# Kernel optimization log

Hardware: AMD Instinct MI355X
Metric: run time of the kernel (lower is better)

## Reference

```python
import jax, jax.numpy as jnp
import numpy as np

N_ENT = 200000   # entity/relation vocab (shared, as code indexes both tables with same ids)
D = 256          # emb_dim
NB = 64          # max neighbors per entity
K = 21           # kernel_num
PROJ = 200       # project_num (hard-coded in module)
S = 5            # few-shot support size
Q = 1024         # query batch
PAD = N_ENT - 1  # padding_idx = len(rel_emb) - 1


def _kernel_mus(k):
    l = [1.0]
    b = 1.0 / (k - 1)
    l.append(1.0 - b / 2.0)
    for i in range(1, k - 1):
        l.append(l[i] - b)
    return np.asarray(l, np.float32)


def _kernel_sigmas(k):
    return np.asarray([0.001] + [0.1] * (k - 1), np.float32)


MU = jnp.asarray(_kernel_mus(K))        # [K]
SIGMA = jnp.asarray(_kernel_sigmas(K))  # [K]


def setup_inputs() -> dict:
    key = jax.random.key(0)
    ks = jax.random.split(key, 12)
    support_heads = jax.random.randint(ks[0], (S,), 0, N_ENT - 1)
    support_tails = jax.random.randint(ks[1], (S,), 0, N_ENT - 1)
    query_heads = jax.random.randint(ks[2], (Q,), 0, N_ENT - 1)
    query_tails = jax.random.randint(ks[3], (Q,), 0, N_ENT - 1)
    raw = jax.random.randint(ks[4], (N_ENT, NB, 2), 0, N_ENT - 1)
    pad_mask = jax.random.uniform(ks[5], (N_ENT, NB, 1)) < 0.2
    edge_data = jnp.where(pad_mask, PAD, raw).astype(jnp.int32)
    edge_nums = jnp.sum(edge_data[..., 1] != PAD, axis=1).astype(jnp.int32)
    rel_emb = jax.random.normal(ks[6], (N_ENT, D), jnp.float32) * 0.02
    ent_emb = jax.random.normal(ks[7], (N_ENT, D), jnp.float32) * 0.02
    sc = 1.0 / np.sqrt(D)
    attn_w = jax.random.normal(ks[8], (D, D), jnp.float32) * sc
    attn_b = jnp.zeros((D,), jnp.float32)
    d1_w = jax.random.normal(ks[9], (PROJ, K), jnp.float32) * (1.0 / np.sqrt(K))
    d1_b = jnp.zeros((PROJ,), jnp.float32)
    d2_w = jax.random.normal(ks[10], (1, PROJ), jnp.float32) * (1.0 / np.sqrt(PROJ))
    d2_b = jnp.zeros((1,), jnp.float32)
    return {
        'support_heads': support_heads, 'query_heads': query_heads,
        'support_tails': support_tails, 'query_tails': query_tails,
        'edge_data': edge_data, 'edge_nums': edge_nums,
        'rel_emb': rel_emb, 'ent_emb': ent_emb,
        'attn_w': attn_w, 'attn_b': attn_b,
        'd1_w': d1_w, 'd1_b': d1_b, 'd2_w': d2_w, 'd2_b': d2_b,
    }


def _l2norm(x):
    # F.normalize(x, 2, dim=-1): x / max(||x||, 1e-12)
    n = jnp.linalg.norm(x, axis=-1, keepdims=True)
    return x / jnp.maximum(n, 1e-12)


def reference(support_heads, query_heads, support_tails, query_tails,
              edge_data, edge_nums, rel_emb, ent_emb,
              attn_w, attn_b, d1_w, d1_b, d2_w, d2_b):
    # neighbor ids (column 1) and padding masks
    s_nb = edge_data[support_tails, :, 1]  # [S, NB]
    q_nb = edge_data[query_tails, :, 1]    # [Q, NB]
    mask_q = (q_nb != PAD).astype(jnp.float32)  # [Q, NB] (mask_s is unused in original)

    def attention(heads, tails, nb):
        t = ent_emb[tails] - ent_emb[heads]          # [B, D] relation-type embed
        t = t @ attn_w.T + attn_b                    # Linear(D, D)
        return jnp.einsum('bd,bnd->bn', t, ent_emb[nb])  # bmm similarity [B, NB]

    s_att = attention(support_heads, support_tails, s_nb)  # [S, NB]
    q_att = attention(query_heads, query_tails, q_nb)      # [Q, NB]

    s_e = _l2norm(rel_emb[s_nb])  # [S, NB, D]
    q_e = _l2norm(rel_emb[q_nb])  # [Q, NB, D]

    # vectorized over the original Python loop on support examples:
    sim = jnp.einsum('qnd,smd->sqnm', q_e, s_e)              # [S, Q, NBq, NBs]
    sim = sim * q_att[None, :, :, None] * s_att[:, None, None, :]
    pool = jnp.max(sim, axis=3)                               # topk(k=1, dim=2) -> [S, Q, NBq]
    pv = jnp.exp(-((pool[..., None] - MU) ** 2) / (SIGMA ** 2) / 2.0)  # [S, Q, NBq, K]
    logpv = jnp.log(jnp.clip(pv, 1e-30, None)) * mask_q[None, :, :, None] * 0.01
    tail_enc = jnp.sum(logpv, axis=2)                         # [S, Q, K]

    h = tail_enc @ d1_w.T + d1_b                              # [S, Q, PROJ]
    score = jax.nn.sigmoid(h @ d2_w.T + d2_b)[..., 0]         # [S, Q]
    return jnp.max(score, axis=0)                             # [Q]
```

## Files before the change

### kernel.cpp

```cpp
#include <hip/hip_runtime.h>
#include <hip/hip_bf16.h>
#include <math.h>

#define N_ENT 200000
#define DD 256
#define NB 64
#define NK 21
#define PROJ 200
#define NS 5
#define NQ 1024
#define PADID (N_ENT - 1)
#define LOGMIN -69.07755279f

typedef short s16x8 __attribute__((ext_vector_type(8)));
typedef float f32x4 __attribute__((ext_vector_type(4)));

__device__ inline unsigned short f2bf(float x) {
  __hip_bfloat16 h = __float2bfloat16(x);
  return __builtin_bit_cast(unsigned short, h);
}

__global__ __launch_bounds__(256) void k_transpose(const float* __restrict__ w,
                                                   float* __restrict__ wT) {
  int j = blockIdx.x, d = threadIdx.x;
  wT[j * DD + d] = w[d * DD + j];
}

__global__ __launch_bounds__(256) void k_t2(const int* __restrict__ qh, const int* __restrict__ qt,
                                            const int* __restrict__ sh, const int* __restrict__ st,
                                            const float* __restrict__ ent, const float* __restrict__ wT,
                                            const float* __restrict__ ab, float* __restrict__ t2) {
  int r = blockIdx.x, d = threadIdx.x;
  int head, tail;
  if (r < NQ) { head = qh[r]; tail = qt[r]; }
  else        { head = sh[r - NQ]; tail = st[r - NQ]; }
  __shared__ float tv[DD];
  tv[d] = ent[(size_t)tail * DD + d] - ent[(size_t)head * DD + d];
  __syncthreads();
  float acc = ab[d];
  #pragma unroll 8
  for (int j = 0; j < DD; ++j) acc += tv[j] * wT[j * DD + d];
  t2[r * DD + d] = acc;
}

__global__ __launch_bounds__(256) void k_qatt(const int* __restrict__ qt, const int* __restrict__ ed,
                                              const float* __restrict__ ent, const float* __restrict__ t2,
                                              float* __restrict__ qatt) {
  int q = blockIdx.x, tid = threadIdx.x;
  __shared__ float t2s[DD];
  __shared__ int nbs[NB];
  t2s[tid] = t2[q * DD + tid];
  if (tid < NB) nbs[tid] = ed[((size_t)qt[q] * NB + tid) * 2 + 1];
  __syncthreads();
  int n = tid >> 2, seg = tid & 3;
  const float4* er = (const float4*)(ent + (size_t)nbs[n] * DD + seg * 64);
  const float4* ts = (const float4*)(t2s + seg * 64);
  float s = 0.f;
  #pragma unroll
  for (int j = 0; j < 16; ++j) {
    float4 v = er[j], t = ts[j];
    s += v.x * t.x + v.y * t.y + v.z * t.z + v.w * t.w;
  }
  s += __shfl_xor(s, 1);
  s += __shfl_xor(s, 2);
  if (seg == 0) qatt[q * NB + n] = s;
}

__global__ __launch_bounds__(256) void k_support(const int* __restrict__ st, const int* __restrict__ ed,
                                                 const float* __restrict__ ent, const float* __restrict__ rel,
                                                 const float* __restrict__ t2,
                                                 unsigned short* __restrict__ Bb) {
  int s = blockIdx.x, tid = threadIdx.x;
  __shared__ float t2s[DD];
  __shared__ int nbs[NB];
  __shared__ float att[NB];
  t2s[tid] = t2[(NQ + s) * DD + tid];
  if (tid < NB) nbs[tid] = ed[((size_t)st[s] * NB + tid) * 2 + 1];
  __syncthreads();
  int n = tid >> 2, seg = tid & 3;
  const float4* er = (const float4*)(ent + (size_t)nbs[n] * DD + seg * 64);
  const float4* ts = (const float4*)(t2s + seg * 64);
  float a = 0.f;
  #pragma unroll
  for (int j = 0; j < 16; ++j) {
    float4 v = er[j], t = ts[j];
    a += v.x * t.x + v.y * t.y + v.z * t.z + v.w * t.w;
  }
  a += __shfl_xor(a, 1);
  a += __shfl_xor(a, 2);
  if (seg == 0) att[n] = a;
  const float4* rr = (const float4*)(rel + (size_t)nbs[n] * DD + seg * 64);
  float4 buf[16];
  float ss = 0.f;
  #pragma unroll
  for (int j = 0; j < 16; ++j) {
    float4 v = rr[j]; buf[j] = v;
    ss += v.x * v.x + v.y * v.y + v.z * v.z + v.w * v.w;
  }
  ss += __shfl_xor(ss, 1);
  ss += __shfl_xor(ss, 2);
  __syncthreads();
  float scale = att[n] / fmaxf(sqrtf(ss), 1e-12f);
  unsigned short* ob = Bb + ((size_t)s * NB + n) * DD + seg * 64;
  #pragma unroll
  for (int j = 0; j < 16; ++j) {
    float4 v = buf[j];
    ob[j * 4 + 0] = f2bf(v.x * scale);
    ob[j * 4 + 1] = f2bf(v.y * scale);
    ob[j * 4 + 2] = f2bf(v.z * scale);
    ob[j * 4 + 3] = f2bf(v.w * scale);
  }
}

#define AP 264
__global__ __launch_bounds__(256) void k_main(
    const int* __restrict__ qt, const int* __restrict__ ed,
    const float* __restrict__ rel, const unsigned short* __restrict__ Bg,
    const float* __restrict__ qatt,
    const float* __restrict__ d1w, const float* __restrict__ d1b,
    const float* __restrict__ d2w, const float* __restrict__ d2b,
    float* __restrict__ out) {
  int q = blockIdx.x, tid = threadIdx.x;
  int wv = tid >> 6, ln = tid & 63;
  int fr = ln & 15, kb = ln >> 4;

  __shared__ __align__(16) unsigned short As[NB * AP];
  __shared__ float pmax[NS][4][NB], pmin[NS][4][NB];
  __shared__ float att[NB], msk[NB], pol[NB], te[NK + 3], wred[4];
  __shared__ int nbs[NB];

  if (tid < NB) {
    int nb = ed[((size_t)qt[q] * NB + tid) * 2 + 1];
    nbs[tid] = nb;
    att[tid] = qatt[q * NB + tid];
    msk[tid] = (nb != PADID) ? 0.01f : 0.0f;
  }
  __syncthreads();
  {
    int n = tid >> 2, seg = tid & 3;
    const float4* rr = (const float4*)(rel + (size_t)nbs[n] * DD + seg * 64);
    float4 buf[16];
    float ss = 0.f;
    #pragma unroll
    for (int j = 0; j < 16; ++j) {
      float4 v = rr[j]; buf[j] = v;
      ss += v.x * v.x + v.y * v.y + v.z * v.z + v.w * v.w;
    }
    ss += __shfl_xor(ss, 1);
    ss += __shfl_xor(ss, 2);
    float inv = 1.0f / fmaxf(sqrtf(ss), 1e-12f);
    unsigned short* ap = As + n * AP + seg * 64;
    #pragma unroll
    for (int j = 0; j < 16; ++j) {
      float4 v = buf[j];
      unsigned int lo = (unsigned int)f2bf(v.x * inv) | ((unsigned int)f2bf(v.y * inv) << 16);
      unsigned int hi = (unsigned int)f2bf(v.z * inv) | ((unsigned int)f2bf(v.w * inv) << 16);
      *(unsigned int*)(ap + j * 4)     = lo;
      *(unsigned int*)(ap + j * 4 + 2) = hi;
    }
  }
  __syncthreads();

  f32x4 acc[4][5];
  #pragma unroll
  for (int i = 0; i < 4; ++i)
    #pragma unroll
    for (int j = 0; j < 5; ++j) acc[i][j] = (f32x4){0.f, 0.f, 0.f, 0.f};

  const unsigned short* abase = As + fr * AP + kb * 8;
  const unsigned short* bbase = Bg + ((size_t)(wv * 16 + fr)) * DD + kb * 8;

  s16x8 bcur[5], bnxt[5], afr[4];
  #pragma unroll
  for (int j = 0; j < 5; ++j) bcur[j] = *(const s16x8*)(bbase + (size_t)j * 64 * DD);
  #pragma unroll
  for (int k = 0; k < 8; ++k) {
    #pragma unroll
    for (int i = 0; i < 4; ++i) afr[i] = *(const s16x8*)(abase + i * 16 * AP + k * 32);
    if (k < 7) {
      #pragma unroll
      for (int j = 0; j < 5; ++j)
        bnxt[j] = *(const s16x8*)(bbase + (size_t)j * 64 * DD + (k + 1) * 32);
    }
    #pragma unroll
    for (int i = 0; i < 4; ++i)
      #pragma unroll
      for (int j = 0; j < 5; ++j)
        acc[i][j] = __builtin_amdgcn_mfma_f32_16x16x32_bf16(afr[i], bcur[j], acc[i][j], 0, 0, 0);
    #pragma unroll
    for (int j = 0; j < 5; ++j) bcur[j] = bnxt[j];
  }

  #pragma unroll
  for (int j = 0; j < 5; ++j) {
    #pragma unroll
    for (int i = 0; i < 4; ++i) {
      f32x4 mx = acc[i][j], mn = acc[i][j];
      #pragma unroll
      for (int off = 1; off < 16; off <<= 1) {
        #pragma unroll
        for (int r2 = 0; r2 < 4; ++r2) {
          mx[r2] = fmaxf(mx[r2], __shfl_xor(mx[r2], off));
          mn[r2] = fminf(mn[r2], __shfl_xor(mn[r2], off));
        }
      }
      if (fr == 0) {
        #pragma unroll
        for (int r2 = 0; r2 < 4; ++r2) {
          pmax[j][wv][i * 16 + kb * 4 + r2] = mx[r2];
          pmin[j][wv][i * 16 + kb * 4 + r2] = mn[r2];
        }
      }
    }
  }
  __syncthreads();

  float lmax = -3.0e38f;
  #pragma unroll 1
  for (int s5 = 0; s5 < NS; ++s5) {
    if (tid < NB) {
      float mx = fmaxf(fmaxf(pmax[s5][0][tid], pmax[s5][1][tid]),
                       fmaxf(pmax[s5][2][tid], pmax[s5][3][tid]));
      float mn = fminf(fminf(pmin[s5][0][tid], pmin[s5][1][tid]),
                       fminf(pmin[s5][2][tid], pmin[s5][3][tid]));
      float qa = att[tid];
      pol[tid] = (qa >= 0.f) ? qa * mx : qa * mn;
    }
    __syncthreads();
    if (tid < NK * 8) {
      int k = tid >> 3, np0 = tid & 7;
      double cur = 1.0;
      if (k >= 1) {
        double bq = 1.0 / (double)(NK - 1);
        cur = 1.0 - bq * 0.5;
        for (int i2 = 1; i2 < k; ++i2) cur -= bq;
      }
      float mu = (float)cur;
      float sig = (k == 0) ? 0.001f : 0.1f;
      float s2 = sig * sig;
      float a = 0.f;
      for (int n = np0; n < NB; n += 8) {
        float dd = pol[n] - mu;
        float x = dd * dd / s2 * 0.5f;
        a += msk[n] * fmaxf(-x, LOGMIN);
      }
      a += __shfl_xor(a, 1);
      a += __shfl_xor(a, 2);
      a += __shfl_xor(a, 4);
      if (np0 == 0) te[k] = a;
    }
    __syncthreads();
    float y = 0.f;
    if (tid < PROJ) {
      float h = d1b[tid];
      #pragma unroll
      for (int k = 0; k < NK; ++k) h += te[k] * d1w[tid * NK + k];
      y = h * d2w[tid];
    }
    #pragma unroll
    for (int off = 1; off < 64; off <<= 1) y += __shfl_xor(y, off);
    if ((tid & 63) == 0) wred[tid >> 6] = y;
    __syncthreads();
    if (tid == 0) {
      float logit = wred[0] + wred[1] + wred[2] + wred[3] + d2b[0];
      lmax = fmaxf(lmax, logit);
    }
  }
  if (tid == 0) out[q] = 1.0f / (1.0f + expf(-lmax));
}

extern "C" void kernel_launch(void* const* d_in, const int* in_sizes, int n_in,
                              void* d_out, int out_size, void* d_ws, size_t ws_size,
                              hipStream_t stream) {
  const int* sh   = (const int*)d_in[0];
  const int* qh   = (const int*)d_in[1];
  const int* st   = (const int*)d_in[2];
  const int* qt   = (const int*)d_in[3];
  const int* ed   = (const int*)d_in[4];
  const float* rel = (const float*)d_in[6];
  const float* ent = (const float*)d_in[7];
  const float* aw  = (const float*)d_in[8];
  const float* ab  = (const float*)d_in[9];
  const float* d1w = (const float*)d_in[10];
  const float* d1b = (const float*)d_in[11];
  const float* d2w = (const float*)d_in[12];
  const float* d2b = (const float*)d_in[13];
  float* out = (float*)d_out;

  float* ws   = (float*)d_ws;
  float* wT   = ws;
  float* t2   = wT + 65536;
  float* qatt = t2 + 263424;
  unsigned short* Bb = (unsigned short*)(qatt + 65536);

  k_transpose<<<DD, DD, 0, stream>>>(aw, wT);
  k_t2<<<NQ + NS, DD, 0, stream>>>(qh, qt, sh, st, ent, wT, ab, t2);
  k_qatt<<<NQ, DD, 0, stream>>>(qt, ed, ent, t2, qatt);
  k_support<<<NS, DD, 0, stream>>>(st, ed, ent, rel, t2, Bb);
  k_main<<<NQ, DD, 0, stream>>>(qt, ed, rel, Bb, qatt, d1w, d1b, d2w, d2b, out);
}
```

Baseline: 484.1 us.

## Fuse attention projection and query attention into the main per-query kernel

Removes the separate t2 and qatt kernels and computes the attention projection (tv @ W^T + b) and the neighbor attention scores inside the main per-query block. The support kernel computes its own projection too. This cuts two launches and the global round-trips for t2 and qatt. The rel-row loads are issued before the projection matvec so their latency overlaps it. The cost is more register pressure and per-block latency in the main kernel.

```diff
diff --git a/kernel.cpp b/kernel.cpp
--- a/kernel.cpp
+++ b/kernel.cpp
@@ -26,56 +26,23 @@
   wT[j * DD + d] = w[d * DD + j];
 }
 
-__global__ __launch_bounds__(256) void k_t2(const int* __restrict__ qh, const int* __restrict__ qt,
-                                            const int* __restrict__ sh, const int* __restrict__ st,
-                                            const float* __restrict__ ent, const float* __restrict__ wT,
-                                            const float* __restrict__ ab, float* __restrict__ t2) {
-  int r = blockIdx.x, d = threadIdx.x;
-  int head, tail;
-  if (r < NQ) { head = qh[r]; tail = qt[r]; }
-  else        { head = sh[r - NQ]; tail = st[r - NQ]; }
-  __shared__ float tv[DD];
-  tv[d] = ent[(size_t)tail * DD + d] - ent[(size_t)head * DD + d];
-  __syncthreads();
-  float acc = ab[d];
-  #pragma unroll 8
-  for (int j = 0; j < DD; ++j) acc += tv[j] * wT[j * DD + d];
-  t2[r * DD + d] = acc;
-}
-
-__global__ __launch_bounds__(256) void k_qatt(const int* __restrict__ qt, const int* __restrict__ ed,
-                                              const float* __restrict__ ent, const float* __restrict__ t2,
-                                              float* __restrict__ qatt) {
-  int q = blockIdx.x, tid = threadIdx.x;
-  __shared__ float t2s[DD];
-  __shared__ int nbs[NB];
-  t2s[tid] = t2[q * DD + tid];
-  if (tid < NB) nbs[tid] = ed[((size_t)qt[q] * NB + tid) * 2 + 1];
-  __syncthreads();
-  int n = tid >> 2, seg = tid & 3;
-  const float4* er = (const float4*)(ent + (size_t)nbs[n] * DD + seg * 64);
-  const float4* ts = (const float4*)(t2s + seg * 64);
-  float s = 0.f;
-  #pragma unroll
-  for (int j = 0; j < 16; ++j) {
-    float4 v = er[j], t = ts[j];
-    s += v.x * t.x + v.y * t.y + v.z * t.z + v.w * t.w;
-  }
-  s += __shfl_xor(s, 1);
-  s += __shfl_xor(s, 2);
-  if (seg == 0) qatt[q * NB + n] = s;
-}
-
-__global__ __launch_bounds__(256) void k_support(const int* __restrict__ st, const int* __restrict__ ed,
+__global__ __launch_bounds__(256) void k_support(const int* __restrict__ sh, const int* __restrict__ st,
+                                                 const int* __restrict__ ed,
                                                  const float* __restrict__ ent, const float* __restrict__ rel,
-                                                 const float* __restrict__ t2,
+                                                 const float* __restrict__ wT, const float* __restrict__ ab,
                                                  unsigned short* __restrict__ Bb) {
   int s = blockIdx.x, tid = threadIdx.x;
-  __shared__ float t2s[DD];
+  __shared__ float tv[DD], t2s[DD];
   __shared__ int nbs[NB];
   __shared__ float att[NB];
-  t2s[tid] = t2[(NQ + s) * DD + tid];
-  if (tid < NB) nbs[tid] = ed[((size_t)st[s] * NB + tid) * 2 + 1];
+  int head = sh[s], tail = st[s];
+  if (tid < NB) nbs[tid] = ed[((size_t)tail * NB + tid) * 2 + 1];
+  tv[tid] = ent[(size_t)tail * DD + tid] - ent[(size_t)head * DD + tid];
+  __syncthreads();
+  float acc0 = ab[tid];
+  #pragma unroll 8
+  for (int j = 0; j < DD; ++j) acc0 = fmaf(tv[j], wT[j * DD + tid], acc0);
+  t2s[tid] = acc0;
   __syncthreads();
   int n = tid >> 2, seg = tid & 3;
   const float4* er = (const float4*)(ent + (size_t)nbs[n] * DD + seg * 64);
@@ -113,10 +80,11 @@
 }
 
 #define AP 264
-__global__ __launch_bounds__(256) void k_main(
-    const int* __restrict__ qt, const int* __restrict__ ed,
-    const float* __restrict__ rel, const unsigned short* __restrict__ Bg,
-    const float* __restrict__ qatt,
+__global__ __launch_bounds__(256) void k_all(
+    const int* __restrict__ qh, const int* __restrict__ qt, const int* __restrict__ ed,
+    const float* __restrict__ ent, const float* __restrict__ rel,
+    const float* __restrict__ wT, const float* __restrict__ ab,
+    const unsigned short* __restrict__ Bg,
     const float* __restrict__ d1w, const float* __restrict__ d1b,
     const float* __restrict__ d2w, const float* __restrict__ d2b,
     float* __restrict__ out) {
@@ -124,26 +92,37 @@
   int wv = tid >> 6, ln = tid & 63;
   int fr = ln & 15, kb = ln >> 4;
 
+  __shared__ float tv[DD], t2s[DD];
   __shared__ __align__(16) unsigned short As[NB * AP];
   __shared__ float pmax[NS][4][NB], pmin[NS][4][NB];
   __shared__ float att[NB], msk[NB], pol[NB], te[NK + 3], wred[4];
   __shared__ int nbs[NB];
 
+  int head = qh[q], tail = qt[q];
   if (tid < NB) {
-    int nb = ed[((size_t)qt[q] * NB + tid) * 2 + 1];
+    int nb = ed[((size_t)tail * NB + tid) * 2 + 1];
     nbs[tid] = nb;
-    att[tid] = qatt[q * NB + tid];
     msk[tid] = (nb != PADID) ? 0.01f : 0.0f;
   }
-  __syncthreads();
+  tv[tid] = ent[(size_t)tail * DD + tid] - ent[(size_t)head * DD + tid];
+  __syncthreads();
+
+  int n = tid >> 2, seg = tid & 3;
+  const float4* rr = (const float4*)(rel + (size_t)nbs[n] * DD + seg * 64);
+  float4 buf[16];
+  #pragma unroll
+  for (int j = 0; j < 16; ++j) buf[j] = rr[j];
+
+  float acc0 = ab[tid];
+  #pragma unroll 8
+  for (int j = 0; j < DD; ++j) acc0 = fmaf(tv[j], wT[j * DD + tid], acc0);
+  t2s[tid] = acc0;
+
   {
-    int n = tid >> 2, seg = tid & 3;
-    const float4* rr = (const float4*)(rel + (size_t)nbs[n] * DD + seg * 64);
-    float4 buf[16];
     float ss = 0.f;
     #pragma unroll
     for (int j = 0; j < 16; ++j) {
-      float4 v = rr[j]; buf[j] = v;
+      float4 v = buf[j];
       ss += v.x * v.x + v.y * v.y + v.z * v.z + v.w * v.w;
     }
     ss += __shfl_xor(ss, 1);
@@ -160,6 +139,20 @@
     }
   }
   __syncthreads();
+
+  {
+    const float4* er = (const float4*)(ent + (size_t)nbs[n] * DD + seg * 64);
+    const float4* ts = (const float4*)(t2s + seg * 64);
+    float a = 0.f;
+    #pragma unroll
+    for (int j = 0; j < 16; ++j) {
+      float4 v = er[j], t = ts[j];
+      a += v.x * t.x + v.y * t.y + v.z * t.z + v.w * t.w;
+    }
+    a += __shfl_xor(a, 1);
+    a += __shfl_xor(a, 2);
+    if (seg == 0) att[n] = a;
+  }
 
   f32x4 acc[4][5];
   #pragma unroll
@@ -239,10 +232,10 @@
       float sig = (k == 0) ? 0.001f : 0.1f;
       float s2 = sig * sig;
       float a = 0.f;
-      for (int n = np0; n < NB; n += 8) {
-        float dd = pol[n] - mu;
+      for (int n2 = np0; n2 < NB; n2 += 8) {
+        float dd = pol[n2] - mu;
         float x = dd * dd / s2 * 0.5f;
-        a += msk[n] * fmaxf(-x, LOGMIN);
+        a += msk[n2] * fmaxf(-x, LOGMIN);
       }
       a += __shfl_xor(a, 1);
       a += __shfl_xor(a, 2);
@@ -287,15 +280,12 @@
   const float* d2b = (const float*)d_in[13];
   float* out = (float*)d_out;
 
-  float* ws   = (float*)d_ws;
-  float* wT   = ws;
-  float* t2   = wT + 65536;
-  float* qatt = t2 + 263424;
-  unsigned short* Bb = (unsigned short*)(qatt + 65536);
+  float* ws = (float*)d_ws;
+  float* wT = ws;
+  unsigned short* Bb = (unsigned short*)(ws + 65536);
 
   k_transpose<<<DD, DD, 0, stream>>>(aw, wT);
-  k_t2<<<NQ + NS, DD, 0, stream>>>(qh, qt, sh, st, ent, wT, ab, t2);
-  k_qatt<<<NQ, DD, 0, stream>>>(qt, ed, ent, t2, qatt);
-  k_support<<<NS, DD, 0, stream>>>(st, ed, ent, rel, t2, Bb);
-  k_main<<<NQ, DD, 0, stream>>>(qt, ed, rel, Bb, qatt, d1w, d1b, d2w, d2b, out);
-}
+  k_support<<<NS, DD, 0, stream>>>(sh, st, ed, ent, rel, wT, ab, Bb);
+  k_all<<<NQ, DD, 0, stream>>>(qh, qt, ed, ent, rel, wT, ab, Bb,
+                               d1w, d1b, d2w, d2b, out);
+}
```

New measurement: 490.3 us. No clear change (+1.3%).
